# Kernel tuning notes

Hardware: AMD Instinct MI355X
Metric: run time of the kernel (lower is better)

The kernel has to match this reference:

```python
import jax, jax.numpy as jnp
import numpy as np

N = 512   # state size
D = 512   # input/output feature size
L = 16384 # sequence length


def setup_inputs() -> dict:
    key = jax.random.key(0)
    kA, kB, kC, ku = jax.random.split(key, 4)
    # Scale/shift A so eigenvalues have negative real part (circular law radius 1,
    # shifted by -1.5) -> stable recurrence over L steps; raw randn(N,N) would overflow.
    A = jax.random.normal(kA, (N, N), dtype=jnp.float32) / np.float32(np.sqrt(N)) - 1.5 * jnp.eye(N, dtype=jnp.float32)
    B = jax.random.normal(kB, (N, D), dtype=jnp.float32)
    C = jax.random.normal(kC, (D, N), dtype=jnp.float32)
    u = jax.random.normal(ku, (L, D), dtype=jnp.float32)
    return {"A": A, "B": B, "C": C, "u": u}


def reference(A, B, C, u):
    # run_SSM with discretization='bilinear' (the default)
    Lseq = u.shape[0]
    n = A.shape[0]
    step = 1.0 / Lseq
    I = jnp.eye(n, dtype=A.dtype)
    BL = jnp.linalg.inv(I - A * (step / 2.0))
    Ab = BL @ (I + A * (step / 2.0))          # [N, N]
    Bb = (BL * step) @ B                       # [N, D]  (torch: BL * step @ B)
    # Precompute Bb @ u_k for all k in one GEMM: [L, N]
    Bu = u @ Bb.T

    def step_fn(x, bu_k):
        x = Ab @ x + bu_k                      # x_{k} = Ab x_{k-1} + Bb u_k
        return x, x

    x0 = jnp.zeros((n,), dtype=A.dtype)
    _, xs = jax.lax.scan(step_fn, x0, Bu)      # xs: [L, N]
    ys = xs @ C.T                              # y_k = Cb x_k -> [L, D]
    return ys
```

## Files before the change

kernel.cpp:

```cpp
#include <hip/hip_runtime.h>
#include <hip/hip_bf16.h>

static constexpr int N = 512;
static constexpr int L = 16384;
static constexpr int SQX = 16;

typedef short s16x8 __attribute__((ext_vector_type(8)));
typedef float f32x4 __attribute__((ext_vector_type(4)));
using bf16 = __hip_bfloat16;

#define GPTR(p) ((const __attribute__((address_space(1))) void*)(p))
#define LPTR(p) ((__attribute__((address_space(3))) void*)(p))
__device__ __forceinline__ void gload16(const void* g, void* l) {
    __builtin_amdgcn_global_load_lds(GPTR(g), LPTR(l), 16, 0, 0);
}

__device__ __forceinline__ void split2(float v, ushort& h, ushort& l) {
    bf16 hb = __float2bfloat16(v);
    h = *reinterpret_cast<ushort*>(&hb);
    bf16 lb = __float2bfloat16(v - __bfloat162float(hb));
    l = *reinterpret_cast<ushort*>(&lb);
}
__device__ __forceinline__ ushort f2h(float v) {
    bf16 hb = __float2bfloat16(v);
    return *reinterpret_cast<ushort*>(&hb);
}
__device__ __forceinline__ float us2f(ushort u) {
    return __bfloat162float(*reinterpret_cast<bf16*>(&u));
}


__global__ void k_zeroinit(int* zb) { zb[blockIdx.x * 256 + threadIdx.x] = 0; }

__global__ void k_prep(const float* __restrict__ A, float* __restrict__ M,
                       float* __restrict__ MT, float h) {
    __shared__ float t[32][33];
    int bx = blockIdx.x * 32, by = blockIdx.y * 32;
    int tx = threadIdx.x, ty = threadIdx.y;
#pragma unroll
    for (int j = 0; j < 32; j += 8) {
        float v = A[(by + ty + j) * N + bx + tx] * h;
        t[ty + j][tx] = v;
        M[(by + ty + j) * N + bx + tx] = v;
    }
    __syncthreads();
#pragma unroll
    for (int j = 0; j < 32; j += 8) MT[(bx + ty + j) * N + by + tx] = t[tx][ty + j];
}

__global__ void k_buildDT(const float* __restrict__ M, const float* __restrict__ M2,
                          bf16* __restrict__ Dh, bf16* __restrict__ Dl,
                          float* __restrict__ DTf, bf16* __restrict__ DTh,
                          bf16* __restrict__ DTl, float* __restrict__ BLm) {
    __shared__ float t[32][33];
    int bx = blockIdx.x * 32, by = blockIdx.y * 32;
    int tx = threadIdx.x, ty = threadIdx.y;
#pragma unroll
    for (int j = 0; j < 32; j += 8) {
        int row = by + ty + j, col = bx + tx;
        size_t off = (size_t)row * N + col;
        float m = M[off], m2 = M2[off];
        float d = 2.0f * (m + m2);
        t[ty + j][tx] = d;
        ushort h, l;
        split2(d, h, l);
        *reinterpret_cast<ushort*>(Dh + off) = h;
        *reinterpret_cast<ushort*>(Dl + off) = l;
        BLm[off] = ((row == col) ? 1.0f : 0.0f) + m + m2;
    }
    __syncthreads();
#pragma unroll
    for (int j = 0; j < 32; j += 8) {
        float v = t[tx][ty + j];
        size_t off = (size_t)(bx + ty + j) * N + by + tx;
        DTf[off] = v;
        ushort h, l;
        split2(v, h, l);
        *reinterpret_cast<ushort*>(DTh + off) = h;
        *reinterpret_cast<ushort*>(DTl + off) = l;
    }
}

__global__ void k_split4(const float* __restrict__ in, bf16* __restrict__ hi,
                         bf16* __restrict__ lo, int n4) {
    int i = blockIdx.x * 256 + threadIdx.x;
    if (i >= n4) return;
    float4 v = reinterpret_cast<const float4*>(in)[i];
    ushort ht[4], lt[4];
    split2(v.x, ht[0], lt[0]);
    split2(v.y, ht[1], lt[1]);
    split2(v.z, ht[2], lt[2]);
    split2(v.w, ht[3], lt[3]);
    *reinterpret_cast<ushort4*>(hi + 4 * (size_t)i) = *reinterpret_cast<ushort4*>(ht);
    *reinterpret_cast<ushort4*>(lo + 4 * (size_t)i) = *reinterpret_cast<ushort4*>(lt);
}

__global__ void k_transpose(const float* __restrict__ in, float* __restrict__ out) {
    __shared__ float t[32][33];
    int bx = blockIdx.x * 32, by = blockIdx.y * 32;
    int tx = threadIdx.x, ty = threadIdx.y;
#pragma unroll
    for (int j = 0; j < 32; j += 8) t[ty + j][tx] = in[(by + ty + j) * N + bx + tx];
    __syncthreads();
#pragma unroll
    for (int j = 0; j < 32; j += 8) out[(bx + ty + j) * N + by + tx] = t[tx][ty + j];
}

__global__ __launch_bounds__(256) void k_qsq(
    const float* __restrict__ Asrc, const float* __restrict__ Bmat,
    float* __restrict__ OUT, bf16* __restrict__ Sh, bf16* __restrict__ Sl, float scale) {
    __shared__ float As[32][64];
    __shared__ float Bs[32][64];
    const int tid = threadIdx.x;
    const int brow = blockIdx.x * 64;
    const int bcol = blockIdx.y * 64;
    const int tx = tid & 15, ty = tid >> 4;
    float acc[4][4] = {};

    for (int k0 = 0; k0 < N; k0 += 32) {
#pragma unroll
        for (int q = 0; q < 2; ++q) {
            int idx = tid * 2 + q;
            int row = idx >> 3;
            int kq = (idx & 7) << 2;
            float4 va = *(const float4*)(Asrc + (long)(brow + row) * N + k0 + kq);
            As[kq + 0][row] = va.x; As[kq + 1][row] = va.y;
            As[kq + 2][row] = va.z; As[kq + 3][row] = va.w;
            float4 vb = *(const float4*)(Bmat + (long)(bcol + row) * N + k0 + kq);
            Bs[kq + 0][row] = vb.x; Bs[kq + 1][row] = vb.y;
            Bs[kq + 2][row] = vb.z; Bs[kq + 3][row] = vb.w;
        }
        __syncthreads();
#pragma unroll
        for (int kk = 0; kk < 32; ++kk) {
            float a[4], b[4];
            *(float4*)&a[0] = *(const float4*)&As[kk][ty * 4];
            *(float4*)&b[0] = *(const float4*)&Bs[kk][tx * 4];
#pragma unroll
            for (int i = 0; i < 4; ++i)
#pragma unroll
                for (int j = 0; j < 4; ++j) acc[i][j] = fmaf(a[i], b[j], acc[i][j]);
        }
        __syncthreads();
    }
#pragma unroll
    for (int i = 0; i < 4; ++i) {
        long off = (long)(brow + ty * 4 + i) * N + bcol + tx * 4;
        float4 o = make_float4(acc[i][0] * scale, acc[i][1] * scale,
                               acc[i][2] * scale, acc[i][3] * scale);
        *(float4*)(OUT + off) = o;
        ushort ht[4], lt[4];
        split2(o.x, ht[0], lt[0]); split2(o.y, ht[1], lt[1]);
        split2(o.z, ht[2], lt[2]); split2(o.w, ht[3], lt[3]);
        *reinterpret_cast<ushort4*>(Sh + off) = *reinterpret_cast<ushort4*>(ht);
        *reinterpret_cast<ushort4*>(Sl + off) = *reinterpret_cast<ushort4*>(lt);
    }
}

__global__ __launch_bounds__(256, 3) void k_bu(
    const float* __restrict__ u, const bf16* __restrict__ Bbh,
    bf16* __restrict__ Xoh)
{
    __shared__ char smem[32768];
    const int tid = threadIdx.x;
    const int wave = tid >> 6, lane = tid & 63;
    const int wm = wave >> 1, wn = wave & 1;
    const int rl = lane & 15, rh = lane >> 4;
    const long brow = (long)blockIdx.x * 128;
    const int bcol = blockIdx.y * 128;

    f32x4 acc[4][4];
#pragma unroll
    for (int m = 0; m < 4; ++m)
#pragma unroll
        for (int n = 0; n < 4; ++n) acc[m][n] = (f32x4){0.f, 0.f, 0.f, 0.f};

    const float* aptr[2]; int awoff[2];
    const char* pB[2]; int wb[2];
#pragma unroll
    for (int q = 0; q < 2; ++q) {
        int idx = q * 256 + tid;
        int row = idx >> 2, slot = idx & 3;
        int sp = slot ^ ((row >> 1) & 3);
        aptr[q] = u + (brow + row) * N + slot * 8;
        awoff[q] = row * 64 + sp * 16;
        pB[q] = (const char*)(Bbh + (long)(bcol + row) * N + sp * 8);
        wb[q] = (q * 256 + wave * 64) * 16;
    }

    auto stageA = [&](int t, char* buf) {
#pragma unroll
        for (int q = 0; q < 2; ++q) {
            f32x4 v0 = *reinterpret_cast<const f32x4*>(aptr[q] + t * 32);
            f32x4 v1 = *reinterpret_cast<const f32x4*>(aptr[q] + t * 32 + 4);
            s16x8 h;
            h[0] = (short)f2h(v0[0]); h[1] = (short)f2h(v0[1]);
            h[2] = (short)f2h(v0[2]); h[3] = (short)f2h(v0[3]);
            h[4] = (short)f2h(v1[0]); h[5] = (short)f2h(v1[1]);
            h[6] = (short)f2h(v1[2]); h[7] = (short)f2h(v1[3]);
            *reinterpret_cast<s16x8*>(buf + awoff[q]) = h;
        }
    };
    auto stageB = [&](int t, char* buf) {
#pragma unroll
        for (int q = 0; q < 2; ++q) gload16(pB[q] + t * 64, buf + 8192 + wb[q]);
    };

    stageA(0, smem);
    stageB(0, smem);
    __syncthreads();

    for (int t = 0; t < 16; ++t) {
        const char* base = smem + (t & 1) * 16384;
        s16x8 a[4], b[4];
#pragma unroll
        for (int m = 0; m < 4; ++m) {
            int row = wm * 64 + m * 16 + rl;
            a[m] = *reinterpret_cast<const s16x8*>(base + row * 64 + (rh ^ ((row >> 1) & 3)) * 16);
        }
#pragma unroll
        for (int n = 0; n < 4; ++n) {
            int row = wn * 64 + n * 16 + rl;
            b[n] = *reinterpret_cast<const s16x8*>(base + 8192 + row * 64 + (rh ^ ((row >> 1) & 3)) * 16);
        }
        if (t + 1 < 16) {
            char* nb = smem + ((t + 1) & 1) * 16384;
            stageA(t + 1, nb);
            stageB(t + 1, nb);
        }
#pragma unroll
        for (int m = 0; m < 4; ++m)
#pragma unroll
            for (int n = 0; n < 4; ++n)
                acc[m][n] = __builtin_amdgcn_mfma_f32_16x16x32_bf16(a[m], b[n], acc[m][n], 0, 0, 0);
        __syncthreads();
    }

    float* eld = (float*)smem;
    const int erow = tid >> 2;
    const int ec   = (tid & 3) * 8;
    for (int h = 0; h < 2; ++h) {
        if (wm == h) {
#pragma unroll
            for (int m = 0; m < 4; ++m)
#pragma unroll
                for (int q = 0; q < 4; ++q) {
                    int br = m * 16 + rh * 4 + q;
                    int sw = (br & 7) << 2;
#pragma unroll
                    for (int n = 0; n < 4; ++n) {
                        int col = wn * 64 + n * 16 + rl;
                        eld[br * 128 + (col ^ sw)] = acc[m][n][q];
                    }
                }
        }
        __syncthreads();
        {
            long gi = brow + h * 64 + erow;
            const int sw = (erow & 7) << 2;
            long gb = gi * N + bcol;
#pragma unroll
            for (int s = 0; s < 4; ++s) {
                int c = ec + s * 32;
                f32x4 v0 = *reinterpret_cast<const f32x4*>(&eld[erow * 128 + (c ^ sw)]);
                f32x4 v1 = *reinterpret_cast<const f32x4*>(&eld[erow * 128 + ((c ^ sw) ^ 4)]);
                float r[8];
                *reinterpret_cast<f32x4*>(&r[0]) = v0;
                *reinterpret_cast<f32x4*>(&r[4]) = v1;
                ushort oh[8];
#pragma unroll
                for (int j = 0; j < 8; ++j) oh[j] = f2h(r[j]);
                *reinterpret_cast<int4*>(Xoh + gb + c) = *reinterpret_cast<int4*>(oh);
            }
        }
        __syncthreads();
    }
}

__global__ __launch_bounds__(256, 3) void k_fin(
    const bf16* __restrict__ Xh, const bf16* __restrict__ Ch, float* __restrict__ Of)
{
    __shared__ char smem[32768];
    const int tid = threadIdx.x;
    const int wave = tid >> 6, lane = tid & 63;
    const int wm = wave >> 1, wn = wave & 1;
    const int rl = lane & 15, rh = lane >> 4;
    const long brow = (long)blockIdx.x * 128;
    const int bcol = blockIdx.y * 128;

    f32x4 acc[4][4];
#pragma unroll
    for (int m = 0; m < 4; ++m)
#pragma unroll
        for (int n = 0; n < 4; ++n) acc[m][n] = (f32x4){0.f, 0.f, 0.f, 0.f};

    const char* pA[2]; const char* pB[2]; int wb[2];
#pragma unroll
    for (int q = 0; q < 2; ++q) {
        int idx = q * 256 + tid;
        int row = idx >> 2, slot = idx & 3;
        int sp = slot ^ ((row >> 1) & 3);
        pA[q] = (const char*)(Xh + (brow + row) * N + sp * 8);
        pB[q] = (const char*)(Ch + (long)(bcol + row) * N + sp * 8);
        wb[q] = (q * 256 + wave * 64) * 16;
    }

#pragma unroll
    for (int q = 0; q < 2; ++q) {
        gload16(pA[q], smem + 0    + wb[q]);
        gload16(pB[q], smem + 8192 + wb[q]);
    }
    __syncthreads();

    for (int t = 0; t < 16; ++t) {
        const char* base = smem + (t & 1) * 16384;
        s16x8 a[4], b[4];
#pragma unroll
        for (int m = 0; m < 4; ++m) {
            int row = wm * 64 + m * 16 + rl;
            a[m] = *reinterpret_cast<const s16x8*>(base + row * 64 + (rh ^ ((row >> 1) & 3)) * 16);
        }
#pragma unroll
        for (int n = 0; n < 4; ++n) {
            int row = wn * 64 + n * 16 + rl;
            b[n] = *reinterpret_cast<const s16x8*>(base + 8192 + row * 64 + (rh ^ ((row >> 1) & 3)) * 16);
        }
        if (t + 1 < 16) {
            const int kb = (t + 1) * 64;
            char* nb = smem + ((t + 1) & 1) * 16384;
#pragma unroll
            for (int q = 0; q < 2; ++q) {
                gload16(pA[q] + kb, nb + 0    + wb[q]);
                gload16(pB[q] + kb, nb + 8192 + wb[q]);
            }
        }
#pragma unroll
        for (int m = 0; m < 4; ++m)
#pragma unroll
            for (int n = 0; n < 4; ++n)
                acc[m][n] = __builtin_amdgcn_mfma_f32_16x16x32_bf16(a[m], b[n], acc[m][n], 0, 0, 0);
        __syncthreads();
    }

    float* eld = (float*)smem;
    const int erow = tid >> 2;
    const int ec   = (tid & 3) * 8;
    for (int h = 0; h < 2; ++h) {
        if (wm == h) {
#pragma unroll
            for (int m = 0; m < 4; ++m)
#pragma unroll
                for (int q = 0; q < 4; ++q) {
                    int br = m * 16 + rh * 4 + q;
                    int sw = (br & 7) << 2;
#pragma unroll
                    for (int n = 0; n < 4; ++n) {
                        int col = wn * 64 + n * 16 + rl;
                        eld[br * 128 + (col ^ sw)] = acc[m][n][q];
                    }
                }
        }
        __syncthreads();
        {
            long gi = brow + h * 64 + erow;
            const int sw = (erow & 7) << 2;
            long gb = gi * N + bcol;
#pragma unroll
            for (int s = 0; s < 4; ++s) {
                int c = ec + s * 32;
                f32x4 v0 = *reinterpret_cast<const f32x4*>(&eld[erow * 128 + (c ^ sw)]);
                f32x4 v1 = *reinterpret_cast<const f32x4*>(&eld[erow * 128 + ((c ^ sw) ^ 4)]);
                *reinterpret_cast<f32x4*>(Of + gb + c)     = v0;
                *reinterpret_cast<f32x4*>(Of + gb + c + 4) = v1;
            }
        }
        __syncthreads();
    }
}

__global__ __launch_bounds__(256, 3) void k_drnd(
    const bf16* __restrict__ Xih, bf16* __restrict__ Xoh,
    const bf16* __restrict__ Dh, const bf16* __restrict__ Dl,
    const bf16* __restrict__ DTh, const bf16* __restrict__ DTl,
    const float* __restrict__ DTf,
    bf16* __restrict__ Dnh, bf16* __restrict__ Dnl,
    bf16* __restrict__ DTnh, bf16* __restrict__ DTnl, float* __restrict__ DTfn,
    int shift, int doSq, const bf16* __restrict__ zb)
{
    __shared__ char smem[32768];
    const int tid = threadIdx.x;
    const int wave = tid >> 6, lane = tid & 63;
    const int wm = wave >> 1, wn = wave & 1;
    const int rl = lane & 15, rh = lane >> 4;

    if (blockIdx.x < SQX) {
        if (!doSq) return;
        int sidx = (int)blockIdx.x * (int)gridDim.y + (int)blockIdx.y;
        const int ti = (sidx >> 3) * 64, tj = (sidx & 7) * 64;

        f32x4 acc[2][2];
#pragma unroll
        for (int m = 0; m < 2; ++m)
#pragma unroll
            for (int n = 0; n < 2; ++n) acc[m][n] = (f32x4){0.f, 0.f, 0.f, 0.f};

        int row = tid >> 2, slot = tid & 3;
        int sp = slot ^ ((row >> 1) & 3);
        const char* pAh = (const char*)(DTh + (size_t)(ti + row) * N + sp * 8);
        const char* pAl = (const char*)(DTl + (size_t)(ti + row) * N + sp * 8);
        const char* pBh = (const char*)(Dh + (size_t)(tj + row) * N + sp * 8);
        const char* pBl = (const char*)(Dl + (size_t)(tj + row) * N + sp * 8);
        const int wb = wave * 1024;

        gload16(pAh, smem + 0     + wb);
        gload16(pAl, smem + 4096  + wb);
        gload16(pBh, smem + 8192  + wb);
        gload16(pBl, smem + 12288 + wb);
        __syncthreads();

        for (int t = 0; t < 16; ++t) {
            const char* base = smem + (t & 1) * 16384;
            s16x8 ah[2], al[2], bh[2], bl[2];
#pragma unroll
            for (int m = 0; m < 2; ++m) {
                int r2 = wm * 32 + m * 16 + rl;
                int off = r2 * 64 + (rh ^ ((r2 >> 1) & 3)) * 16;
                ah[m] = *reinterpret_cast<const s16x8*>(base + off);
                al[m] = *reinterpret_cast<const s16x8*>(base + 4096 + off);
            }
#pragma unroll
            for (int n = 0; n < 2; ++n) {
                int r2 = wn * 32 + n * 16 + rl;
                int off = r2 * 64 + (rh ^ ((r2 >> 1) & 3)) * 16;
                bh[n] = *reinterpret_cast<const s16x8*>(base + 8192 + off);
                bl[n] = *reinterpret_cast<const s16x8*>(base + 12288 + off);
            }
            if (t + 1 < 16) {
                const int kb = (t + 1) * 64;
                char* nb = smem + ((t + 1) & 1) * 16384;
                gload16(pAh + kb, nb + 0     + wb);
                gload16(pAl + kb, nb + 4096  + wb);
                gload16(pBh + kb, nb + 8192  + wb);
                gload16(pBl + kb, nb + 12288 + wb);
            }
#pragma unroll
            for (int m = 0; m < 2; ++m)
#pragma unroll
                for (int n = 0; n < 2; ++n) {
                    acc[m][n] = __builtin_amdgcn_mfma_f32_16x16x32_bf16(ah[m], bh[n], acc[m][n], 0, 0, 0);
                    acc[m][n] = __builtin_amdgcn_mfma_f32_16x16x32_bf16(ah[m], bl[n], acc[m][n], 0, 0, 0);
                    acc[m][n] = __builtin_amdgcn_mfma_f32_16x16x32_bf16(al[m], bh[n], acc[m][n], 0, 0, 0);
                }
            __syncthreads();
        }

#pragma unroll
        for (int m = 0; m < 2; ++m)
#pragma unroll
            for (int n = 0; n < 2; ++n)
#pragma unroll
                for (int q = 0; q < 4; ++q) {
                    int i = ti + wm * 32 + m * 16 + rh * 4 + q;
                    int j = tj + wn * 32 + n * 16 + rl;
                    size_t off = (size_t)i * N + j;
                    float v = acc[m][n][q] + 2.0f * DTf[off];
                    DTfn[off] = v;
                    ushort h, l;
                    split2(v, h, l);
                    *reinterpret_cast<ushort*>(DTnh + off) = h;
                    *reinterpret_cast<ushort*>(DTnl + off) = l;
                    size_t offT = (size_t)j * N + i;
                    *reinterpret_cast<ushort*>(Dnh + offT) = h;
                    *reinterpret_cast<ushort*>(Dnl + offT) = l;
                }
        return;
    }

    int bigbx = (int)blockIdx.x - SQX;
    const int sb = shift >> 7;
    int rowBlk = bigbx + sb;
    bool isCopy = false;
    if (rowBlk >= (L / 128)) { rowBlk -= (L / 128); isCopy = true; }
    const long brow = (long)rowBlk * 128;
    const int bcol = blockIdx.y * 128;

    if (isCopy) {
#pragma unroll
        for (int j = 0; j < 8; ++j) {
            int c = j * 256 + tid;
            long off = (brow + (c >> 4)) * N + bcol + (c & 15) * 8;
            *reinterpret_cast<int4*>(Xoh + off) = *reinterpret_cast<const int4*>(Xih + off);
        }
        return;
    }

    f32x4 acc[4][4];
#pragma unroll
    for (int m = 0; m < 4; ++m)
#pragma unroll
        for (int n = 0; n < 4; ++n) acc[m][n] = (f32x4){0.f, 0.f, 0.f, 0.f};

    const char* pA[2]; const char* pB[2]; int wb[2];
#pragma unroll
    for (int q = 0; q < 2; ++q) {
        int idx = q * 256 + tid;
        int row = idx >> 2, slot = idx & 3;
        int sp = slot ^ ((row >> 1) & 3);
        long gra = brow + row - (long)shift;
        pA[q] = (gra >= 0) ? (const char*)(Xih + gra * N + sp * 8)
                           : (const char*)(zb + sp * 8);
        pB[q] = (const char*)(Dh + (long)(bcol + row) * N + sp * 8);
        wb[q] = (q * 256 + wave * 64) * 16;
    }

#pragma unroll
    for (int q = 0; q < 2; ++q) {
        gload16(pA[q], smem + 0    + wb[q]);
        gload16(pB[q], smem + 8192 + wb[q]);
    }
    __syncthreads();

    for (int t = 0; t < 16; ++t) {
        const char* base = smem + (t & 1) * 16384;
        s16x8 a[4], b[4];
#pragma unroll
        for (int m = 0; m < 4; ++m) {
            int row = wm * 64 + m * 16 + rl;
            a[m] = *reinterpret_cast<const s16x8*>(base + row * 64 + (rh ^ ((row >> 1) & 3)) * 16);
        }
#pragma unroll
        for (int n = 0; n < 4; ++n) {
            int row = wn * 64 + n * 16 + rl;
            b[n] = *reinterpret_cast<const s16x8*>(base + 8192 + row * 64 + (rh ^ ((row >> 1) & 3)) * 16);
        }
        if (t + 1 < 16) {
            const int kb = (t + 1) * 64;
            char* nb = smem + ((t + 1) & 1) * 16384;
#pragma unroll
            for (int q = 0; q < 2; ++q) {
                gload16(pA[q] + kb, nb + 0    + wb[q]);
                gload16(pB[q] + kb, nb + 8192 + wb[q]);
            }
        }
#pragma unroll
        for (int m = 0; m < 4; ++m)
#pragma unroll
            for (int n = 0; n < 4; ++n)
                acc[m][n] = __builtin_amdgcn_mfma_f32_16x16x32_bf16(a[m], b[n], acc[m][n], 0, 0, 0);
        __syncthreads();
    }

    float* eld = (float*)smem;
    const int erow = tid >> 2;
    const int ec   = (tid & 3) * 8;
    for (int h = 0; h < 2; ++h) {
        if (wm == h) {
#pragma unroll
            for (int m = 0; m < 4; ++m)
#pragma unroll
                for (int q = 0; q < 4; ++q) {
                    int br = m * 16 + rh * 4 + q;
                    int sw = (br & 7) << 2;
#pragma unroll
                    for (int n = 0; n < 4; ++n) {
                        int col = wn * 64 + n * 16 + rl;
                        eld[br * 128 + (col ^ sw)] = acc[m][n][q];
                    }
                }
        }
        __syncthreads();
        {
            long gi = brow + h * 64 + erow;
            bool hasS = gi >= (long)shift;
            const int sw = (erow & 7) << 2;
            long gb = gi * N + bcol;
            long gs = gb - (long)shift * N;
#pragma unroll
            for (int s = 0; s < 4; ++s) {
                int c = ec + s * 32;
                f32x4 v0 = *reinterpret_cast<const f32x4*>(&eld[erow * 128 + (c ^ sw)]);
                f32x4 v1 = *reinterpret_cast<const f32x4*>(&eld[erow * 128 + ((c ^ sw) ^ 4)]);
                float r[8];
                *reinterpret_cast<f32x4*>(&r[0]) = v0;
                *reinterpret_cast<f32x4*>(&r[4]) = v1;
                ushort vh[8];
                *reinterpret_cast<int4*>(vh) = *reinterpret_cast<const int4*>(Xih + gb + c);
#pragma unroll
                for (int j = 0; j < 8; ++j) r[j] += us2f(vh[j]);
                if (hasS) {
                    *reinterpret_cast<int4*>(vh) = *reinterpret_cast<const int4*>(Xih + gs + c);
#pragma unroll
                    for (int j = 0; j < 8; ++j) r[j] += us2f(vh[j]);
                }
                ushort oh[8];
#pragma unroll
                for (int j = 0; j < 8; ++j) oh[j] = f2h(r[j]);
                *reinterpret_cast<int4*>(Xoh + gb + c) = *reinterpret_cast<int4*>(oh);
            }
        }
        __syncthreads();
    }
}


extern "C" void kernel_launch(void* const* d_in, const int* in_sizes, int n_in,
                              void* d_out, int out_size, void* d_ws, size_t ws_size,
                              hipStream_t stream) {
    (void)in_sizes; (void)n_in; (void)out_size; (void)ws_size;
    const float* A = (const float*)d_in[0];
    const float* B = (const float*)d_in[1];
    const float* C = (const float*)d_in[2];
    const float* u = (const float*)d_in[3];

    const size_t NN = (size_t)N * N;
    const size_t LN = (size_t)L * N;

    bf16* X1h = (bf16*)d_out;

    char* w = (char*)d_ws;
    bf16* X0h = (bf16*)w;      w += LN * 2;
    bf16 *Dh_[2], *Dl_[2], *DTh_[2], *DTl_[2];
    float* DTf_[2];
    for (int s = 0; s < 2; ++s) {
        Dh_[s]  = (bf16*)w;    w += NN * 2;
        Dl_[s]  = (bf16*)w;    w += NN * 2;
        DTh_[s] = (bf16*)w;    w += NN * 2;
        DTl_[s] = (bf16*)w;    w += NN * 2;
        DTf_[s] = (float*)w;   w += NN * 4;
    }
    float* M   = (float*)w;    w += NN * 4;
    float* MT  = (float*)w;    w += NN * 4;
    float* M2  = (float*)w;    w += NN * 4;
    float* BLm = (float*)w;    w += NN * 4;
    float* BT  = (float*)w;    w += NN * 4;
    float* Bbf = (float*)w;    w += NN * 4;
    bf16* Bbh  = (bf16*)w;     w += NN * 2;
    bf16* Bbl  = (bf16*)w;     w += NN * 2;
    bf16* Ch   = (bf16*)w;     w += NN * 2;
    bf16* Cl   = (bf16*)w;     w += NN * 2;
    bf16* zb   = (bf16*)w;     w += 2048;

    const float step = 1.0f / (float)L;

    dim3 b256(256);
    dim3 bT(32, 8), gT(N / 32, N / 32);
    dim3 g64(N / 64, N / 64);
    dim3 gBig(L / 128, N / 128);
    dim3 gRound(SQX + L / 128, N / 128);
    dim3 gS4n((int)(NN / 4 / 256));

    k_zeroinit<<<2, 256, 0, stream>>>((int*)zb);

    k_prep<<<gT, bT, 0, stream>>>(A, M, MT, step * 0.5f);
    k_qsq<<<g64, b256, 0, stream>>>(M, MT, M2, Bbh, Bbl, 1.0f);
    k_buildDT<<<gT, bT, 0, stream>>>(M, M2, Dh_[0], Dl_[0],
                                     DTf_[0], DTh_[0], DTl_[0], BLm);
    k_transpose<<<gT, bT, 0, stream>>>(B, BT);
    k_qsq<<<g64, b256, 0, stream>>>(BLm, BT, Bbf, Bbh, Bbl, step);
    k_split4<<<gS4n, b256, 0, stream>>>(C, Ch, Cl, (int)(NN / 4));

    k_bu<<<gBig, b256, 0, stream>>>(u, Bbh, X0h);

    for (int r = 0; r < 14; ++r) {
        int s = r & 1, nx = s ^ 1;
        bf16* Xih = (r & 1) ? X1h : X0h;
        bf16* Xoh = (r & 1) ? X0h : X1h;
        int doSq = (r < 13) ? 1 : 0;
        k_drnd<<<gRound, b256, 0, stream>>>(
            Xih, Xoh, Dh_[s], Dl_[s],
            DTh_[s], DTl_[s], DTf_[s],
            Dh_[nx], Dl_[nx], DTh_[nx], DTl_[nx], DTf_[nx], 1 << r, doSq, zb);
    }

    k_fin<<<gBig, b256, 0, stream>>>(X0h, Ch, (float*)d_out);
}
```

Measured before the change: 386.3 us.

## Keep finalized prefix rows in a separate buffer to skip copy blocks in doubling rounds

Rows already final after each doubling round are now written to a dedicated buffer F instead of being copied from the input to the output ping-pong buffer. This removes the copy blocks, and the grid shrinks by the finished row-blocks in later rounds. Reads of shifted rows pick F or the ping-pong buffer depending on whether the row is finalized. The final GEMM reads from F. It costs an extra L×N bf16 workspace buffer and more complex indexing, with a risk of stale or missed rows at the boundaries.

After: 394.2 us. 1.02x slower.

```diff
diff --git a/kernel.cpp b/kernel.cpp
--- a/kernel.cpp
+++ b/kernel.cpp
@@ -380,6 +380,7 @@
 
 __global__ __launch_bounds__(256, 3) void k_drnd(
     const bf16* __restrict__ Xih, bf16* __restrict__ Xoh,
+    const bf16* __restrict__ Fin, bf16* __restrict__ Fout,
     const bf16* __restrict__ Dh, const bf16* __restrict__ Dl,
     const bf16* __restrict__ DTh, const bf16* __restrict__ DTl,
     const float* __restrict__ DTf,
@@ -476,23 +477,9 @@
         return;
     }
 
-    int bigbx = (int)blockIdx.x - SQX;
     const int sb = shift >> 7;
-    int rowBlk = bigbx + sb;
-    bool isCopy = false;
-    if (rowBlk >= (L / 128)) { rowBlk -= (L / 128); isCopy = true; }
-    const long brow = (long)rowBlk * 128;
+    const long brow = (long)((int)blockIdx.x - SQX + sb) * 128;
     const int bcol = blockIdx.y * 128;
-
-    if (isCopy) {
-#pragma unroll
-        for (int j = 0; j < 8; ++j) {
-            int c = j * 256 + tid;
-            long off = (brow + (c >> 4)) * N + bcol + (c & 15) * 8;
-            *reinterpret_cast<int4*>(Xoh + off) = *reinterpret_cast<const int4*>(Xih + off);
-        }
-        return;
-    }
 
     f32x4 acc[4][4];
 #pragma unroll
@@ -507,8 +494,11 @@
         int row = idx >> 2, slot = idx & 3;
         int sp = slot ^ ((row >> 1) & 3);
         long gra = brow + row - (long)shift;
-        pA[q] = (gra >= 0) ? (const char*)(Xih + gra * N + sp * 8)
-                           : (const char*)(zb + sp * 8);
+        const char* src;
+        if (gra < 0)                 src = (const char*)(zb + sp * 8);
+        else if (gra < (long)shift)  src = (const char*)(Fin + gra * N + sp * 8);
+        else                         src = (const char*)(Xih + gra * N + sp * 8);
+        pA[q] = src;
         pB[q] = (const char*)(Dh + (long)(bcol + row) * N + sp * 8);
         wb[q] = (q * 256 + wave * 64) * 16;
     }
@@ -571,31 +561,37 @@
         __syncthreads();
         {
             long gi = brow + h * 64 + erow;
-            bool hasS = gi >= (long)shift;
-            const int sw = (erow & 7) << 2;
-            long gb = gi * N + bcol;
-            long gs = gb - (long)shift * N;
-#pragma unroll
-            for (int s = 0; s < 4; ++s) {
-                int c = ec + s * 32;
-                f32x4 v0 = *reinterpret_cast<const f32x4*>(&eld[erow * 128 + (c ^ sw)]);
-                f32x4 v1 = *reinterpret_cast<const f32x4*>(&eld[erow * 128 + ((c ^ sw) ^ 4)]);
-                float r[8];
-                *reinterpret_cast<f32x4*>(&r[0]) = v0;
-                *reinterpret_cast<f32x4*>(&r[4]) = v1;
-                ushort vh[8];
-                *reinterpret_cast<int4*>(vh) = *reinterpret_cast<const int4*>(Xih + gb + c);
-#pragma unroll
-                for (int j = 0; j < 8; ++j) r[j] += us2f(vh[j]);
-                if (hasS) {
-                    *reinterpret_cast<int4*>(vh) = *reinterpret_cast<const int4*>(Xih + gs + c);
+            bool active = (gi >= (long)shift) || (shift == 1);
+            if (active) {
+                bool hasS = gi >= (long)shift;
+                long gs = gi - (long)shift;
+                const bf16* xs = (gs < (long)shift) ? Fin : Xih;
+                bf16* tgt = (gi < 2 * (long)shift) ? Fout : Xoh;
+                const int sw = (erow & 7) << 2;
+                long gb = gi * N + bcol;
+                long gsb = gs * N + bcol;
+#pragma unroll
+                for (int s = 0; s < 4; ++s) {
+                    int c = ec + s * 32;
+                    f32x4 v0 = *reinterpret_cast<const f32x4*>(&eld[erow * 128 + (c ^ sw)]);
+                    f32x4 v1 = *reinterpret_cast<const f32x4*>(&eld[erow * 128 + ((c ^ sw) ^ 4)]);
+                    float r[8];
+                    *reinterpret_cast<f32x4*>(&r[0]) = v0;
+                    *reinterpret_cast<f32x4*>(&r[4]) = v1;
+                    ushort vh[8];
+                    *reinterpret_cast<int4*>(vh) = *reinterpret_cast<const int4*>(Xih + gb + c);
 #pragma unroll
                     for (int j = 0; j < 8; ++j) r[j] += us2f(vh[j]);
+                    if (hasS) {
+                        *reinterpret_cast<int4*>(vh) = *reinterpret_cast<const int4*>(xs + gsb + c);
+#pragma unroll
+                        for (int j = 0; j < 8; ++j) r[j] += us2f(vh[j]);
+                    }
+                    ushort oh[8];
+#pragma unroll
+                    for (int j = 0; j < 8; ++j) oh[j] = f2h(r[j]);
+                    *reinterpret_cast<int4*>(tgt + gb + c) = *reinterpret_cast<int4*>(oh);
                 }
-                ushort oh[8];
-#pragma unroll
-                for (int j = 0; j < 8; ++j) oh[j] = f2h(r[j]);
-                *reinterpret_cast<int4*>(Xoh + gb + c) = *reinterpret_cast<int4*>(oh);
             }
         }
         __syncthreads();
@@ -619,6 +615,7 @@
 
     char* w = (char*)d_ws;
     bf16* X0h = (bf16*)w;      w += LN * 2;
+    bf16* F   = (bf16*)w;      w += LN * 2;
     bf16 *Dh_[2], *Dl_[2], *DTh_[2], *DTl_[2];
     float* DTf_[2];
     for (int s = 0; s < 2; ++s) {
@@ -646,7 +643,6 @@
     dim3 bT(32, 8), gT(N / 32, N / 32);
     dim3 g64(N / 64, N / 64);
     dim3 gBig(L / 128, N / 128);
-    dim3 gRound(SQX + L / 128, N / 128);
     dim3 gS4n((int)(NN / 4 / 256));
 
     k_zeroinit<<<2, 256, 0, stream>>>((int*)zb);
@@ -665,12 +661,15 @@
         int s = r & 1, nx = s ^ 1;
         bf16* Xih = (r & 1) ? X1h : X0h;
         bf16* Xoh = (r & 1) ? X0h : X1h;
+        const bf16* Fin = (r == 0) ? (const bf16*)X0h : (const bf16*)F;
         int doSq = (r < 13) ? 1 : 0;
+        int sb = (r >= 7) ? (1 << (r - 7)) : 0;
+        dim3 gRound(SQX + L / 128 - sb, N / 128);
         k_drnd<<<gRound, b256, 0, stream>>>(
-            Xih, Xoh, Dh_[s], Dl_[s],
+            Xih, Xoh, Fin, F, Dh_[s], Dl_[s],
             DTh_[s], DTl_[s], DTf_[s],
             Dh_[nx], Dl_[nx], DTh_[nx], DTl_[nx], DTf_[nx], 1 << r, doSq, zb);
     }
 
-    k_fin<<<gBig, b256, 0, stream>>>(X0h, Ch, (float*)d_out);
-}
+    k_fin<<<gBig, b256, 0, stream>>>(F, Ch, (float*)d_out);
+}
```
